# Optimization experiments

Measured on AMD Instinct MI355X. Metric: run time of the kernel, lower is better.

## Reference

```python
import jax, jax.numpy as jnp
import numpy as np

N, E, H, NH, D, T, L = 50000, 800000, 128, 8, 16, 6, 2  # nodes, edges, hidden, heads, head_dim, node types, layers


def setup_inputs() -> dict:
    key = jax.random.key(0)
    ks = jax.random.split(key, 16)
    s = 1.0 / np.sqrt(H)
    return {
        "hidden": jax.random.normal(ks[0], (N, H), jnp.float32),
        "cn": jax.random.normal(ks[1], (N, H), jnp.float32),
        "x_norm_abs": jax.random.uniform(ks[2], (N, 2), jnp.float32),
        "node_type": jax.random.randint(ks[3], (N,), 0, T, jnp.int32),
        "edge_src": jax.random.randint(ks[4], (E,), 0, N, jnp.int32),
        "edge_dst": jax.random.randint(ks[5], (E,), 0, N, jnp.int32),
        # learned params, stacked over L layers (num_relations=1 folded out)
        "W_pos": jax.random.normal(ks[6], (L, 2, H), jnp.float32) * 0.1,
        "Wk": jax.random.normal(ks[7], (L, T, H, H), jnp.float32) * s,
        "Wq": jax.random.normal(ks[8], (L, T, H, H), jnp.float32) * s,
        "Wv": jax.random.normal(ks[9], (L, T, H, H), jnp.float32) * s,
        "Wa": jax.random.normal(ks[10], (L, T, H, H), jnp.float32) * s,
        "rel_att": jax.random.normal(ks[11], (L, NH, D, D), jnp.float32) * (1.0 / np.sqrt(D)),
        "rel_msg": jax.random.normal(ks[12], (L, NH, D, D), jnp.float32) * (1.0 / np.sqrt(D)),
        "rel_pri": jnp.ones((L, NH), jnp.float32),
        "skip": jnp.zeros((L, T), jnp.float32),
        "w_pri": jax.random.normal(ks[13], (L, H), jnp.float32) * s,
    }


def reference(hidden, cn, x_norm_abs, node_type, edge_src, edge_dst,
              W_pos, Wk, Wq, Wv, Wa, rel_att, rel_msg, rel_pri, skip, w_pri):
    n, h_dim = hidden.shape
    nh, d = rel_att.shape[1], rel_att.shape[2]
    inv_sqrt_d = 1.0 / np.sqrt(d)
    ar = jnp.arange(n)
    priority = jnp.zeros((n,), hidden.dtype)

    for l in range(Wk.shape[0]):  # small fixed layer count
        h = hidden + x_norm_abs @ W_pos[l]                      # positional injection of x_norm_abs

        def per_type(W):
            all_t = jnp.einsum('nh,thd->tnd', h, W)             # [T,N,H] per-node-type projections
            return all_t[node_type, ar].reshape(n, nh, d)       # select own type -> [N,NH,D]

        k, q, v = per_type(Wk[l]), per_type(Wq[l]), per_type(Wv[l])
        ke, qe, ve = k[edge_src], q[edge_dst], v[edge_src]      # [E,NH,D] irregular gathers

        att = jnp.einsum('ehd,hdf,ehf->eh', ke, rel_att[l], qe) * rel_pri[l] * inv_sqrt_d
        amax = jax.ops.segment_max(att, edge_dst, num_segments=n)
        ex = jnp.exp(att - amax[edge_dst])
        den = jax.ops.segment_sum(ex, edge_dst, num_segments=n)
        alpha = ex / (den[edge_dst] + 1e-16)                    # per-destination softmax over edges

        msg = jnp.einsum('ehd,hdf->ehf', ve, rel_msg[l]) * alpha[..., None]
        agg = jax.ops.segment_sum(msg.reshape(-1, nh * d), edge_dst, num_segments=n)  # [N,H]

        trans = jax.nn.gelu(agg)
        out_all = jnp.einsum('nh,thd->tnd', trans, Wa[l])
        out = out_all[node_type, ar]
        sk = jax.nn.sigmoid(skip[l])[node_type][:, None]
        hgt_out = sk * out + (1.0 - sk) * h

        priority = jax.nn.sigmoid(hgt_out @ w_pri[l])
        cn = hgt_out + cn                                       # cn_now = hgt_out + cn_now
        hidden = hidden + jnp.tanh(cn)                          # hidden = hidden + tanh(cn)

    return hidden, cn, priority
```

## Files before the change

### kernel.cpp

```cpp
#include <hip/hip_runtime.h>
#include <hip/hip_bf16.h>
#include <math.h>

#define N_NODES 50000
#define N_EDGES 800000
#define HID     128
#define NHEAD   8
#define HDIM    16
#define NTYPE   6
#define NLAYER  2
#define TILE_N  64
#define PROJ_BLOCKS_PER_TYPE 782

typedef unsigned int uint_;
typedef unsigned short ushort_;

__device__ __forceinline__ float sigmoidf_(float x){ return 1.f/(1.f+__expf(-x)); }
__device__ __forceinline__ float gelu_tanh(float x){
  float x3 = x*x*x;
  return 0.5f*x*(1.f + tanhf(0.7978845608028654f*(x + 0.044715f*x3)));
}
__device__ __forceinline__ uint_ pack_bf2(float lo, float hi){
  union{float f; uint_ u;} a, b; a.f = lo; b.f = hi;
  uint_ ua = (a.u + 0x7FFFu + ((a.u >> 16) & 1u)) >> 16;
  uint_ ub = (b.u + 0x7FFFu + ((b.u >> 16) & 1u)) & 0xFFFF0000u;
  return ua | ub;
}

__global__ void k_hist(const int* __restrict__ edst, int* __restrict__ deg){
  int e = blockIdx.x*256 + threadIdx.x;
  if (e < N_EDGES) atomicAdd(&deg[edst[e]], 1);
}

__global__ void __launch_bounds__(1024)
k_scan(const int* __restrict__ deg, int* __restrict__ rowptr){
  __shared__ int part[1024];
  const int chunk = (N_NODES + 1023)/1024;
  int t = threadIdx.x;
  int beg = t*chunk, end = min(beg+chunk, N_NODES);
  int s = 0;
  for (int i = beg; i < end; ++i) s += deg[i];
  part[t] = s;
  __syncthreads();
  if (t == 0){
    int acc = 0;
    for (int i = 0; i < 1024; ++i){ int v = part[i]; part[i] = acc; acc += v; }
    rowptr[N_NODES] = acc;
  }
  __syncthreads();
  int acc = part[t];
  for (int i = beg; i < end; ++i){ rowptr[i] = acc; acc += deg[i]; }
}

__global__ void k_fill(const int* __restrict__ esrc, const int* __restrict__ edst,
                       const int* __restrict__ rowptr, int* __restrict__ cursor,
                       int* __restrict__ csr_src){
  int e = blockIdx.x*256 + threadIdx.x;
  if (e < N_EDGES){
    int d = edst[e];
    int pos = atomicAdd(&cursor[d], 1);
    csr_src[rowptr[d] + pos] = esrc[e];
  }
}

__global__ void k_thist(const int* __restrict__ ntype, int* __restrict__ tcount){
  __shared__ int c[NTYPE];
  int t = threadIdx.x;
  if (t < NTYPE) c[t] = 0;
  __syncthreads();
  int n = blockIdx.x*256 + t;
  if (n < N_NODES) atomicAdd(&c[ntype[n]], 1);
  __syncthreads();
  if (t < NTYPE && c[t] > 0) atomicAdd(&tcount[t], c[t]);
}

__global__ void k_tscan(const int* __restrict__ tcount, int* __restrict__ toffset){
  if (threadIdx.x == 0){
    int acc = 0;
    for (int i = 0; i < NTYPE; ++i){ toffset[i] = acc; acc += tcount[i]; }
  }
}

__global__ void k_tfill(const int* __restrict__ ntype, const int* __restrict__ toffset,
                        int* __restrict__ tcursor, int* __restrict__ tnodes){
  __shared__ int c[NTYPE], base[NTYPE];
  int t = threadIdx.x;
  if (t < NTYPE) c[t] = 0;
  __syncthreads();
  int n = blockIdx.x*256 + t;
  int ty = 0, rank = 0;
  bool valid = (n < N_NODES);
  if (valid){ ty = ntype[n]; rank = atomicAdd(&c[ty], 1); }
  __syncthreads();
  if (t < NTYPE && c[t] > 0) base[t] = atomicAdd(&tcursor[t], c[t]);
  __syncthreads();
  if (valid) tnodes[toffset[ty] + base[ty] + rank] = n;
}

__global__ void k_effw(const float* __restrict__ Wk, const float* __restrict__ Wv,
                       const float* __restrict__ A, const float* __restrict__ M,
                       const float* __restrict__ pri, float* __restrict__ WkA,
                       float* __restrict__ WvM){
  int idx = blockIdx.x*256 + threadIdx.x;
  if (idx >= NTYPE*HID*HID) return;
  int hf = idx & (HID-1);
  int hh = hf >> 4, f = hf & 15;
  int base = idx - hf;
  const float* a  = A + hh*HDIM*HDIM;
  const float* m  = M + hh*HDIM*HDIM;
  const float* wk = Wk + base + hh*HDIM;
  const float* wv = Wv + base + hh*HDIM;
  float sa = 0.f, sm = 0.f;
  #pragma unroll
  for (int d = 0; d < HDIM; ++d){ sa += wk[d]*a[d*HDIM+f]; sm += wv[d]*m[d*HDIM+f]; }
  WkA[idx] = sa * pri[hh] * 0.25f;
  WvM[idx] = sm;
}

__global__ void __launch_bounds__(256)
k_proj_t(const float* __restrict__ hidden, const float* __restrict__ xnorm,
         const int* __restrict__ tnodes, const int* __restrict__ tcount,
         const int* __restrict__ toffset, const float* __restrict__ Wpos,
         const float* __restrict__ Wq, const float* __restrict__ WkA,
         const float* __restrict__ WvM, float* __restrict__ qout,
         ushort_* __restrict__ kvout){
  int bid  = blockIdx.x;
  int m    = bid % 3;
  int rest = bid / 3;
  int ty   = rest / PROJ_BLOCKS_PER_TYPE;
  int tile = rest % PROJ_BLOCKS_PER_TYPE;
  int cnt  = tcount[ty];
  int base = tile*TILE_N;
  if (base >= cnt) return;
  __shared__ float hs[TILE_N][HID];
  __shared__ int nl[TILE_N];
  int t  = threadIdx.x;
  int c  = t & 31;
  int rt = t >> 5;
  int off = toffset[ty];
  float4 w0 = *(const float4*)(Wpos + 4*c);
  float4 w1 = *(const float4*)(Wpos + HID + 4*c);
  #pragma unroll
  for (int pass = 0; pass < 8; ++pass){
    int r = pass*8 + rt;
    int node = -1;
    float4 hv = make_float4(0.f,0.f,0.f,0.f);
    if (base + r < cnt){
      node = tnodes[off + base + r];
      float xa0 = xnorm[2*node], xa1 = xnorm[2*node+1];
      float4 hd = *(const float4*)(hidden + (size_t)node*HID + 4*c);
      hv.x = hd.x + xa0*w0.x + xa1*w1.x;
      hv.y = hd.y + xa0*w0.y + xa1*w1.y;
      hv.z = hd.z + xa0*w0.z + xa1*w1.z;
      hv.w = hd.w + xa0*w0.w + xa1*w1.w;
    }
    if (c == 0) nl[r] = node;
    *(float4*)&hs[r][4*c] = hv;
  }
  __syncthreads();

  const float* W = (m == 0 ? Wq : (m == 1 ? WkA : WvM)) + (size_t)ty*HID*HID;
  float4 acc[8];
  #pragma unroll
  for (int r = 0; r < 8; ++r) acc[r] = make_float4(0.f,0.f,0.f,0.f);
  for (int k0 = 0; k0 < HID; k0 += 4){
    float4 hr[8];
    #pragma unroll
    for (int r = 0; r < 8; ++r) hr[r] = *(const float4*)&hs[rt*8+r][k0];
    #pragma unroll
    for (int kk = 0; kk < 4; ++kk){
      float4 w = *(const float4*)(W + (size_t)(k0+kk)*HID + 4*c);
      #pragma unroll
      for (int r = 0; r < 8; ++r){
        float hvv = ((const float*)&hr[r])[kk];
        acc[r].x = fmaf(hvv, w.x, acc[r].x);
        acc[r].y = fmaf(hvv, w.y, acc[r].y);
        acc[r].z = fmaf(hvv, w.z, acc[r].z);
        acc[r].w = fmaf(hvv, w.w, acc[r].w);
      }
    }
  }
  #pragma unroll
  for (int r = 0; r < 8; ++r){
    int node = nl[rt*8+r];
    if (node >= 0){
      if (m == 0){
        *(float4*)(qout + (size_t)node*HID + 4*c) = acc[r];
      } else {
        uint2 pk = make_uint2(pack_bf2(acc[r].x, acc[r].y),
                              pack_bf2(acc[r].z, acc[r].w));
        size_t o = (size_t)node*2*HID + (m == 2 ? HID : 0) + 4*c;
        *(uint2*)(kvout + o) = pk;
      }
    }
  }
}

__global__ void k_edge(const int* __restrict__ rowptr, const int* __restrict__ csr_src,
                       const float* __restrict__ q, const ushort_* __restrict__ kv,
                       float* __restrict__ trans){
  int wid = threadIdx.x >> 6, lane = threadIdx.x & 63;
  int n = blockIdx.x*4 + wid;
  int j = 2*lane;
  int beg = rowptr[n], end = rowptr[n+1];
  float2 qv = *(const float2*)(q + (size_t)n*HID + j);
  float m = -INFINITY, s = 0.f, a0 = 0.f, a1 = 0.f;
  int e = beg;
  for (; e + 4 <= end; e += 4){
    uint_ kb[4], vb[4];
    float p[4];
    #pragma unroll
    for (int u = 0; u < 4; ++u){
      const ushort_* r0 = kv + (size_t)csr_src[e+u]*2*HID + j;
      kb[u] = *(const uint_*)r0;
      vb[u] = *(const uint_*)(r0 + HID);
    }
    #pragma unroll
    for (int u = 0; u < 4; ++u){
      float kx = __uint_as_float(kb[u] << 16);
      float ky = __uint_as_float(kb[u] & 0xFFFF0000u);
      float pp = kx*qv.x + ky*qv.y;
      pp += __shfl_xor(pp,1); pp += __shfl_xor(pp,2); pp += __shfl_xor(pp,4);
      p[u] = pp;
    }
    float mn = fmaxf(fmaxf(p[0],p[1]), fmaxf(p[2],p[3]));
    mn = fmaxf(m, mn);
    float fct = __expf(m - mn);
    s *= fct; a0 *= fct; a1 *= fct;
    #pragma unroll
    for (int u = 0; u < 4; ++u){
      float w = __expf(p[u] - mn);
      float vx = __uint_as_float(vb[u] << 16);
      float vy = __uint_as_float(vb[u] & 0xFFFF0000u);
      s += w; a0 = fmaf(w, vx, a0); a1 = fmaf(w, vy, a1);
    }
    m = mn;
  }
  for (; e < end; ++e){
    const ushort_* r0 = kv + (size_t)csr_src[e]*2*HID + j;
    uint_ kb = *(const uint_*)r0;
    uint_ vb = *(const uint_*)(r0 + HID);
    float kx = __uint_as_float(kb << 16);
    float ky = __uint_as_float(kb & 0xFFFF0000u);
    float pp = kx*qv.x + ky*qv.y;
    pp += __shfl_xor(pp,1); pp += __shfl_xor(pp,2); pp += __shfl_xor(pp,4);
    float mn  = fmaxf(m, pp);
    float fct = __expf(m - mn);
    float w   = __expf(pp - mn);
    float vx = __uint_as_float(vb << 16);
    float vy = __uint_as_float(vb & 0xFFFF0000u);
    s  = s*fct + w;
    a0 = fmaf(w, vx, a0*fct);
    a1 = fmaf(w, vy, a1*fct);
    m = mn;
  }
  float inv = 1.f/(s + 1e-16f);
  *(float2*)(trans + (size_t)n*HID + j) =
      make_float2(gelu_tanh(a0*inv), gelu_tanh(a1*inv));
}

__global__ void __launch_bounds__(256)
k_post_t(const float* __restrict__ trans, const float* __restrict__ xnorm,
         const int* __restrict__ tnodes, const int* __restrict__ tcount,
         const int* __restrict__ toffset, const float* __restrict__ Wpos,
         const float* __restrict__ Wa, const float* __restrict__ skip,
         const float* __restrict__ wpri,
         const float* __restrict__ hsrc, const float* __restrict__ csrc,
         float* __restrict__ hdst, float* __restrict__ cdst,
         float* __restrict__ pri, int last){
  int ty   = blockIdx.x / PROJ_BLOCKS_PER_TYPE;
  int tile = blockIdx.x % PROJ_BLOCKS_PER_TYPE;
  int cnt  = tcount[ty];
  int base = tile*TILE_N;
  if (base >= cnt) return;
  __shared__ float ts[TILE_N][HID];
  __shared__ int nl[TILE_N];
  int t  = threadIdx.x;
  int c  = t & 31;
  int rt = t >> 5;
  int off = toffset[ty];
  #pragma unroll
  for (int pass = 0; pass < 8; ++pass){
    int r = pass*8 + rt;
    int node = -1;
    float4 tv = make_float4(0.f,0.f,0.f,0.f);
    if (base + r < cnt){
      node = tnodes[off + base + r];
      tv = *(const float4*)(trans + (size_t)node*HID + 4*c);
    }
    if (c == 0) nl[r] = node;
    *(float4*)&ts[r][4*c] = tv;
  }
  __syncthreads();

  const float* W = Wa + (size_t)ty*HID*HID;
  float4 acc[8];
  #pragma unroll
  for (int r = 0; r < 8; ++r) acc[r] = make_float4(0.f,0.f,0.f,0.f);
  for (int k0 = 0; k0 < HID; k0 += 4){
    float4 hr[8];
    #pragma unroll
    for (int r = 0; r < 8; ++r) hr[r] = *(const float4*)&ts[rt*8+r][k0];
    #pragma unroll
    for (int kk = 0; kk < 4; ++kk){
      float4 w = *(const float4*)(W + (size_t)(k0+kk)*HID + 4*c);
      #pragma unroll
      for (int r = 0; r < 8; ++r){
        float hvv = ((const float*)&hr[r])[kk];
        acc[r].x = fmaf(hvv, w.x, acc[r].x);
        acc[r].y = fmaf(hvv, w.y, acc[r].y);
        acc[r].z = fmaf(hvv, w.z, acc[r].z);
        acc[r].w = fmaf(hvv, w.w, acc[r].w);
      }
    }
  }

  float sk = sigmoidf_(skip[ty]);
  float4 w0 = *(const float4*)(Wpos + 4*c);
  float4 w1 = *(const float4*)(Wpos + HID + 4*c);
  float4 wp = *(const float4*)(wpri + 4*c);
  float ppv[8];
  #pragma unroll
  for (int r = 0; r < 8; ++r){
    int node = nl[rt*8+r];
    ppv[r] = 0.f;
    if (node < 0) continue;
    size_t o = (size_t)node*HID + 4*c;
    float xa0 = xnorm[2*node], xa1 = xnorm[2*node+1];
    float4 hd = *(const float4*)(hsrc + o);
    float4 cv = *(const float4*)(csrc + o);
    float h0 = hd.x + xa0*w0.x + xa1*w1.x;
    float h1 = hd.y + xa0*w0.y + xa1*w1.y;
    float h2 = hd.z + xa0*w0.z + xa1*w1.z;
    float h3 = hd.w + xa0*w0.w + xa1*w1.w;
    float hg0 = sk*acc[r].x + (1.f - sk)*h0;
    float hg1 = sk*acc[r].y + (1.f - sk)*h1;
    float hg2 = sk*acc[r].z + (1.f - sk)*h2;
    float hg3 = sk*acc[r].w + (1.f - sk)*h3;
    ppv[r] = hg0*wp.x + hg1*wp.y + hg2*wp.z + hg3*wp.w;
    float c0 = hg0 + cv.x, c1 = hg1 + cv.y, c2 = hg2 + cv.z, c3 = hg3 + cv.w;
    *(float4*)(cdst + o) = make_float4(c0, c1, c2, c3);
    *(float4*)(hdst + o) = make_float4(hd.x + tanhf(c0), hd.y + tanhf(c1),
                                       hd.z + tanhf(c2), hd.w + tanhf(c3));
  }
  if (last){
    #pragma unroll
    for (int r = 0; r < 8; ++r){
      float pp = ppv[r];
      pp += __shfl_xor(pp, 1); pp += __shfl_xor(pp, 2); pp += __shfl_xor(pp, 4);
      pp += __shfl_xor(pp, 8); pp += __shfl_xor(pp, 16);
      ppv[r] = pp;
    }
    if (c == 0){
      #pragma unroll
      for (int r = 0; r < 8; ++r){
        int node = nl[rt*8+r];
        if (node >= 0) pri[node] = sigmoidf_(ppv[r]);
      }
    }
  }
}

extern "C" void kernel_launch(void* const* d_in, const int* in_sizes, int n_in,
                              void* d_out, int out_size, void* d_ws, size_t ws_size,
                              hipStream_t stream){
  const float* hidden_in = (const float*)d_in[0];
  const float* cn_in     = (const float*)d_in[1];
  const float* xnorm     = (const float*)d_in[2];
  const int*   ntype     = (const int*)d_in[3];
  const int*   esrc      = (const int*)d_in[4];
  const int*   edst      = (const int*)d_in[5];
  const float* Wpos      = (const float*)d_in[6];
  const float* Wk        = (const float*)d_in[7];
  const float* Wq        = (const float*)d_in[8];
  const float* Wv        = (const float*)d_in[9];
  const float* Wa        = (const float*)d_in[10];
  const float* Ratt      = (const float*)d_in[11];
  const float* Rmsg      = (const float*)d_in[12];
  const float* Rpri      = (const float*)d_in[13];
  const float* Skip      = (const float*)d_in[14];
  const float* Wpri      = (const float*)d_in[15];

  char* ws = (char*)d_ws;
  size_t off = 0;
  auto alloc = [&](size_t bytes)->void*{ void* p = ws + off; off += (bytes + 255) & ~(size_t)255; return p; };
  float*   qbuf  = (float*)alloc((size_t)N_NODES*HID*4);
  ushort_* kvbuf = (ushort_*)alloc((size_t)N_NODES*2*HID*2);
  float* WkA   = (float*)alloc((size_t)NTYPE*HID*HID*4);
  float* WvM   = (float*)alloc((size_t)NTYPE*HID*HID*4);
  int* deg     = (int*)alloc((size_t)N_NODES*4);
  int* rowptr  = (int*)alloc((size_t)(N_NODES+1)*4);
  int* cursor  = (int*)alloc((size_t)N_NODES*4);
  int* csr     = (int*)alloc((size_t)N_EDGES*4);
  int* tcount  = (int*)alloc(8*4);
  int* toffset = (int*)alloc(8*4);
  int* tcursor = (int*)alloc(8*4);
  int* tnodes  = (int*)alloc((size_t)N_NODES*4);

  float* out_hidden = (float*)d_out;
  float* out_cn     = out_hidden + (size_t)N_NODES*HID;
  float* out_pri    = out_cn     + (size_t)N_NODES*HID;

  hipMemsetAsync(deg,     0, (size_t)N_NODES*4, stream);
  hipMemsetAsync(cursor,  0, (size_t)N_NODES*4, stream);
  hipMemsetAsync(tcount,  0, 8*4, stream);
  hipMemsetAsync(tcursor, 0, 8*4, stream);
  k_hist<<<(N_EDGES+255)/256, 256, 0, stream>>>(edst, deg);
  k_scan<<<1, 1024, 0, stream>>>(deg, rowptr);
  k_fill<<<(N_EDGES+255)/256, 256, 0, stream>>>(esrc, edst, rowptr, cursor, csr);
  k_thist<<<(N_NODES+255)/256, 256, 0, stream>>>(ntype, tcount);
  k_tscan<<<1, 64, 0, stream>>>(tcount, toffset);
  k_tfill<<<(N_NODES+255)/256, 256, 0, stream>>>(ntype, toffset, tcursor, tnodes);

  const int proj_grid = 3 * NTYPE * PROJ_BLOCKS_PER_TYPE;
  const int post_grid = NTYPE * PROJ_BLOCKS_PER_TYPE;
  for (int l = 0; l < NLAYER; ++l){
    const float* Wpos_l = Wpos + (size_t)l*2*HID;
    const float* Wq_l   = Wq   + (size_t)l*NTYPE*HID*HID;
    const float* Wk_l   = Wk   + (size_t)l*NTYPE*HID*HID;
    const float* Wv_l   = Wv   + (size_t)l*NTYPE*HID*HID;
    const float* Wa_l   = Wa   + (size_t)l*NTYPE*HID*HID;
    const float* Ratt_l = Ratt + (size_t)l*NHEAD*HDIM*HDIM;
    const float* Rmsg_l = Rmsg + (size_t)l*NHEAD*HDIM*HDIM;
    const float* Rpri_l = Rpri + (size_t)l*NHEAD;
    const float* Skip_l = Skip + (size_t)l*NTYPE;
    const float* Wpri_l = Wpri + (size_t)l*HID;

    const float* hsrc = (l == 0) ? hidden_in : out_hidden;
    const float* csrc = (l == 0) ? cn_in     : out_cn;

    k_effw<<<(NTYPE*HID*HID+255)/256, 256, 0, stream>>>(Wk_l, Wv_l, Ratt_l, Rmsg_l, Rpri_l, WkA, WvM);
    k_proj_t<<<proj_grid, 256, 0, stream>>>(hsrc, xnorm, tnodes, tcount, toffset,
                                            Wpos_l, Wq_l, WkA, WvM, qbuf, kvbuf);
    k_edge<<<N_NODES/4, 256, 0, stream>>>(rowptr, csr, qbuf, kvbuf, qbuf);
    k_post_t<<<post_grid, 256, 0, stream>>>(qbuf, xnorm, tnodes, tcount, toffset,
                                            Wpos_l, Wa_l, Skip_l, Wpri_l,
                                            hsrc, csrc, out_hidden, out_cn,
                                            out_pri, l == NLAYER-1);
  }
}
```

Measured before the change: 675.9 us.

## Use bf16 MFMA for per-type projection and output GEMMs with prepacked weights

Replaces the scalar FP32 shared-memory GEMMs in the projection and post kernels with bf16 MFMA 16x16x32 instructions. A new weight-pack kernel folds the relation matrices into Wk and Wv, converts all four weight sets to bf16, and stores them in MFMA fragment order. The projection kernel now does q, k and v in one block, so activations are loaded once instead of three times. The risks are reduced precision from bf16 inputs and more scattered, narrower stores (per-element writes across node rows) in place of float4 writes.

```diff
diff --git a/kernel.cpp b/kernel.cpp
--- a/kernel.cpp
+++ b/kernel.cpp
@@ -9,22 +9,21 @@
 #define HDIM    16
 #define NTYPE   6
 #define NLAYER  2
-#define TILE_N  64
-#define PROJ_BLOCKS_PER_TYPE 782
+#define PBT     782
 
 typedef unsigned int uint_;
 typedef unsigned short ushort_;
+typedef __attribute__((ext_vector_type(4))) float f32x4;
+typedef __attribute__((ext_vector_type(8))) short short8;
 
 __device__ __forceinline__ float sigmoidf_(float x){ return 1.f/(1.f+__expf(-x)); }
 __device__ __forceinline__ float gelu_tanh(float x){
   float x3 = x*x*x;
   return 0.5f*x*(1.f + tanhf(0.7978845608028654f*(x + 0.044715f*x3)));
 }
-__device__ __forceinline__ uint_ pack_bf2(float lo, float hi){
-  union{float f; uint_ u;} a, b; a.f = lo; b.f = hi;
-  uint_ ua = (a.u + 0x7FFFu + ((a.u >> 16) & 1u)) >> 16;
-  uint_ ub = (b.u + 0x7FFFu + ((b.u >> 16) & 1u)) & 0xFFFF0000u;
-  return ua | ub;
+__device__ __forceinline__ ushort_ bf16r(float x){
+  union{float f; uint_ u;} v; v.f = x;
+  return (ushort_)((v.u + 0x7FFFu + ((v.u >> 16) & 1u)) >> 16);
 }
 
 __global__ void k_hist(const int* __restrict__ edst, int* __restrict__ deg){
@@ -97,100 +96,113 @@
   if (valid) tnodes[toffset[ty] + base[ty] + rank] = n;
 }
 
-__global__ void k_effw(const float* __restrict__ Wk, const float* __restrict__ Wv,
-                       const float* __restrict__ A, const float* __restrict__ M,
-                       const float* __restrict__ pri, float* __restrict__ WkA,
-                       float* __restrict__ WvM){
+__global__ void k_packw(const float* __restrict__ Wq, const float* __restrict__ Wk,
+                        const float* __restrict__ Wv, const float* __restrict__ Wa,
+                        const float* __restrict__ A,  const float* __restrict__ M,
+                        const float* __restrict__ pri, uint4* __restrict__ wpk){
   int idx = blockIdx.x*256 + threadIdx.x;
-  if (idx >= NTYPE*HID*HID) return;
-  int hf = idx & (HID-1);
-  int hh = hf >> 4, f = hf & 15;
-  int base = idx - hf;
-  const float* a  = A + hh*HDIM*HDIM;
-  const float* m  = M + hh*HDIM*HDIM;
-  const float* wk = Wk + base + hh*HDIM;
-  const float* wv = Wv + base + hh*HDIM;
-  float sa = 0.f, sm = 0.f;
-  #pragma unroll
-  for (int d = 0; d < HDIM; ++d){ sa += wk[d]*a[d*HDIM+f]; sm += wv[d]*m[d*HDIM+f]; }
-  WkA[idx] = sa * pri[hh] * 0.25f;
-  WvM[idx] = sm;
+  if (idx >= NTYPE*4*4*8*64) return;
+  int l  = idx & 63;
+  int ct = (idx >> 6) & 7;
+  int ks = (idx >> 9) & 3;
+  int m  = (idx >> 11) & 3;
+  int t  = idx >> 13;
+  int kbase = ks*32 + (l >> 4)*8;
+  int c15 = l & 15;
+  ushort_ out[8];
+  if (m == 0 || m == 3){
+    const float* W = (m == 0 ? Wq : Wa) + (size_t)t*HID*HID;
+    int col = ct*16 + c15;
+    #pragma unroll
+    for (int j = 0; j < 8; ++j) out[j] = bf16r(W[(size_t)(kbase+j)*HID + col]);
+  } else {
+    const float* W = (m == 1 ? Wk : Wv) + (size_t)t*HID*HID;
+    const float* R = (m == 1 ? A : M) + ct*HDIM*HDIM;
+    float scale = (m == 1) ? pri[ct]*0.25f : 1.f;
+    #pragma unroll
+    for (int j = 0; j < 8; ++j){
+      const float* wrow = W + (size_t)(kbase+j)*HID + ct*16;
+      float s = 0.f;
+      #pragma unroll
+      for (int d = 0; d < HDIM; ++d) s += wrow[d]*R[d*HDIM + c15];
+      out[j] = bf16r(s*scale);
+    }
+  }
+  uint4 pk;
+  pk.x = (uint_)out[0] | ((uint_)out[1] << 16);
+  pk.y = (uint_)out[2] | ((uint_)out[3] << 16);
+  pk.z = (uint_)out[4] | ((uint_)out[5] << 16);
+  pk.w = (uint_)out[6] | ((uint_)out[7] << 16);
+  wpk[idx] = pk;
 }
 
 __global__ void __launch_bounds__(256)
-k_proj_t(const float* __restrict__ hidden, const float* __restrict__ xnorm,
+k_proj_t(const float* __restrict__ hsrc, const float* __restrict__ xnorm,
          const int* __restrict__ tnodes, const int* __restrict__ tcount,
          const int* __restrict__ toffset, const float* __restrict__ Wpos,
-         const float* __restrict__ Wq, const float* __restrict__ WkA,
-         const float* __restrict__ WvM, float* __restrict__ qout,
+         const uint4* __restrict__ wpk, float* __restrict__ qout,
          ushort_* __restrict__ kvout){
-  int bid  = blockIdx.x;
-  int m    = bid % 3;
-  int rest = bid / 3;
-  int ty   = rest / PROJ_BLOCKS_PER_TYPE;
-  int tile = rest % PROJ_BLOCKS_PER_TYPE;
+  int ty   = blockIdx.x / PBT;
+  int tile = blockIdx.x % PBT;
   int cnt  = tcount[ty];
-  int base = tile*TILE_N;
-  if (base >= cnt) return;
-  __shared__ float hs[TILE_N][HID];
-  __shared__ int nl[TILE_N];
-  int t  = threadIdx.x;
-  int c  = t & 31;
-  int rt = t >> 5;
+  int wid  = threadIdx.x >> 6, l = threadIdx.x & 63;
+  int rowbase = tile*64 + wid*16;
+  if (rowbase >= cnt) return;
   int off = toffset[ty];
-  float4 w0 = *(const float4*)(Wpos + 4*c);
-  float4 w1 = *(const float4*)(Wpos + HID + 4*c);
+  int l15 = l & 15, lk = l >> 4;
+
+  int nrowA = rowbase + l15;
+  int nodeA = tnodes[off + (nrowA < cnt ? nrowA : 0)];
+  float xa0 = xnorm[2*nodeA], xa1 = xnorm[2*nodeA+1];
+  short8 afr[4];
   #pragma unroll
-  for (int pass = 0; pass < 8; ++pass){
-    int r = pass*8 + rt;
-    int node = -1;
-    float4 hv = make_float4(0.f,0.f,0.f,0.f);
-    if (base + r < cnt){
-      node = tnodes[off + base + r];
-      float xa0 = xnorm[2*node], xa1 = xnorm[2*node+1];
-      float4 hd = *(const float4*)(hidden + (size_t)node*HID + 4*c);
-      hv.x = hd.x + xa0*w0.x + xa1*w1.x;
-      hv.y = hd.y + xa0*w0.y + xa1*w1.y;
-      hv.z = hd.z + xa0*w0.z + xa1*w1.z;
-      hv.w = hd.w + xa0*w0.w + xa1*w1.w;
-    }
-    if (c == 0) nl[r] = node;
-    *(float4*)&hs[r][4*c] = hv;
-  }
-  __syncthreads();
-
-  const float* W = (m == 0 ? Wq : (m == 1 ? WkA : WvM)) + (size_t)ty*HID*HID;
-  float4 acc[8];
+  for (int ks = 0; ks < 4; ++ks){
+    int col = ks*32 + lk*8;
+    float4 h0 = *(const float4*)(hsrc + (size_t)nodeA*HID + col);
+    float4 h1 = *(const float4*)(hsrc + (size_t)nodeA*HID + col + 4);
+    float4 p0 = *(const float4*)(Wpos + col);
+    float4 p1 = *(const float4*)(Wpos + col + 4);
+    float4 q0 = *(const float4*)(Wpos + HID + col);
+    float4 q1 = *(const float4*)(Wpos + HID + col + 4);
+    union{ ushort_ h[8]; short8 s; } ap;
+    ap.h[0] = bf16r(h0.x + xa0*p0.x + xa1*q0.x);
+    ap.h[1] = bf16r(h0.y + xa0*p0.y + xa1*q0.y);
+    ap.h[2] = bf16r(h0.z + xa0*p0.z + xa1*q0.z);
+    ap.h[3] = bf16r(h0.w + xa0*p0.w + xa1*q0.w);
+    ap.h[4] = bf16r(h1.x + xa0*p1.x + xa1*q1.x);
+    ap.h[5] = bf16r(h1.y + xa0*p1.y + xa1*q1.y);
+    ap.h[6] = bf16r(h1.z + xa0*p1.z + xa1*q1.z);
+    ap.h[7] = bf16r(h1.w + xa0*p1.w + xa1*q1.w);
+    afr[ks] = ap.s;
+  }
+
+  int  ndw[4]; bool nvw[4];
   #pragma unroll
-  for (int r = 0; r < 8; ++r) acc[r] = make_float4(0.f,0.f,0.f,0.f);
-  for (int k0 = 0; k0 < HID; k0 += 4){
-    float4 hr[8];
-    #pragma unroll
-    for (int r = 0; r < 8; ++r) hr[r] = *(const float4*)&hs[rt*8+r][k0];
-    #pragma unroll
-    for (int kk = 0; kk < 4; ++kk){
-      float4 w = *(const float4*)(W + (size_t)(k0+kk)*HID + 4*c);
+  for (int reg = 0; reg < 4; ++reg){
+    int nr = rowbase + lk*4 + reg;
+    nvw[reg] = (nr < cnt);
+    ndw[reg] = tnodes[off + (nvw[reg] ? nr : 0)];
+  }
+
+  #pragma unroll 1
+  for (int m = 0; m < 3; ++m){
+    const uint4* wb = wpk + ((size_t)(ty*4 + m)*32)*64;
+    #pragma unroll 1
+    for (int ct = 0; ct < 8; ++ct){
+      f32x4 acc = {0.f, 0.f, 0.f, 0.f};
       #pragma unroll
-      for (int r = 0; r < 8; ++r){
-        float hvv = ((const float*)&hr[r])[kk];
-        acc[r].x = fmaf(hvv, w.x, acc[r].x);
-        acc[r].y = fmaf(hvv, w.y, acc[r].y);
-        acc[r].z = fmaf(hvv, w.z, acc[r].z);
-        acc[r].w = fmaf(hvv, w.w, acc[r].w);
+      for (int ks = 0; ks < 4; ++ks){
+        union{ uint4 u; short8 s; } bw;
+        bw.u = wb[(ks*8 + ct)*64 + l];
+        acc = __builtin_amdgcn_mfma_f32_16x16x32_bf16(afr[ks], bw.s, acc, 0, 0, 0);
       }
-    }
-  }
-  #pragma unroll
-  for (int r = 0; r < 8; ++r){
-    int node = nl[rt*8+r];
-    if (node >= 0){
-      if (m == 0){
-        *(float4*)(qout + (size_t)node*HID + 4*c) = acc[r];
-      } else {
-        uint2 pk = make_uint2(pack_bf2(acc[r].x, acc[r].y),
-                              pack_bf2(acc[r].z, acc[r].w));
-        size_t o = (size_t)node*2*HID + (m == 2 ? HID : 0) + 4*c;
-        *(uint2*)(kvout + o) = pk;
+      int colw = ct*16 + l15;
+      #pragma unroll
+      for (int reg = 0; reg < 4; ++reg){
+        if (nvw[reg]){
+          if (m == 0) qout[(size_t)ndw[reg]*HID + colw] = acc[reg];
+          else kvout[(size_t)ndw[reg]*2*HID + (m == 2 ? HID : 0) + colw] = bf16r(acc[reg]);
+        }
       }
     }
   }
@@ -263,100 +275,77 @@
 k_post_t(const float* __restrict__ trans, const float* __restrict__ xnorm,
          const int* __restrict__ tnodes, const int* __restrict__ tcount,
          const int* __restrict__ toffset, const float* __restrict__ Wpos,
-         const float* __restrict__ Wa, const float* __restrict__ skip,
+         const uint4* __restrict__ wpk, const float* __restrict__ skip,
          const float* __restrict__ wpri,
          const float* __restrict__ hsrc, const float* __restrict__ csrc,
          float* __restrict__ hdst, float* __restrict__ cdst,
          float* __restrict__ pri, int last){
-  int ty   = blockIdx.x / PROJ_BLOCKS_PER_TYPE;
-  int tile = blockIdx.x % PROJ_BLOCKS_PER_TYPE;
+  int ty   = blockIdx.x / PBT;
+  int tile = blockIdx.x % PBT;
   int cnt  = tcount[ty];
-  int base = tile*TILE_N;
-  if (base >= cnt) return;
-  __shared__ float ts[TILE_N][HID];
-  __shared__ int nl[TILE_N];
-  int t  = threadIdx.x;
-  int c  = t & 31;
-  int rt = t >> 5;
+  int wid  = threadIdx.x >> 6, l = threadIdx.x & 63;
+  int rowbase = tile*64 + wid*16;
+  if (rowbase >= cnt) return;
   int off = toffset[ty];
+  int l15 = l & 15, lk = l >> 4;
+
+  int nrowA = rowbase + l15;
+  int nodeA = tnodes[off + (nrowA < cnt ? nrowA : 0)];
+  short8 afr[4];
   #pragma unroll
-  for (int pass = 0; pass < 8; ++pass){
-    int r = pass*8 + rt;
-    int node = -1;
-    float4 tv = make_float4(0.f,0.f,0.f,0.f);
-    if (base + r < cnt){
-      node = tnodes[off + base + r];
-      tv = *(const float4*)(trans + (size_t)node*HID + 4*c);
-    }
-    if (c == 0) nl[r] = node;
-    *(float4*)&ts[r][4*c] = tv;
-  }
-  __syncthreads();
-
-  const float* W = Wa + (size_t)ty*HID*HID;
-  float4 acc[8];
-  #pragma unroll
-  for (int r = 0; r < 8; ++r) acc[r] = make_float4(0.f,0.f,0.f,0.f);
-  for (int k0 = 0; k0 < HID; k0 += 4){
-    float4 hr[8];
-    #pragma unroll
-    for (int r = 0; r < 8; ++r) hr[r] = *(const float4*)&ts[rt*8+r][k0];
-    #pragma unroll
-    for (int kk = 0; kk < 4; ++kk){
-      float4 w = *(const float4*)(W + (size_t)(k0+kk)*HID + 4*c);
-      #pragma unroll
-      for (int r = 0; r < 8; ++r){
-        float hvv = ((const float*)&hr[r])[kk];
-        acc[r].x = fmaf(hvv, w.x, acc[r].x);
-        acc[r].y = fmaf(hvv, w.y, acc[r].y);
-        acc[r].z = fmaf(hvv, w.z, acc[r].z);
-        acc[r].w = fmaf(hvv, w.w, acc[r].w);
+  for (int ks = 0; ks < 4; ++ks){
+    int col = ks*32 + lk*8;
+    float4 t0 = *(const float4*)(trans + (size_t)nodeA*HID + col);
+    float4 t1 = *(const float4*)(trans + (size_t)nodeA*HID + col + 4);
+    union{ ushort_ h[8]; short8 s; } ap;
+    ap.h[0] = bf16r(t0.x); ap.h[1] = bf16r(t0.y);
+    ap.h[2] = bf16r(t0.z); ap.h[3] = bf16r(t0.w);
+    ap.h[4] = bf16r(t1.x); ap.h[5] = bf16r(t1.y);
+    ap.h[6] = bf16r(t1.z); ap.h[7] = bf16r(t1.w);
+    afr[ks] = ap.s;
+  }
+
+  const uint4* wb = wpk + ((size_t)(ty*4 + 3)*32)*64;
+  f32x4 accs[8];
+  #pragma unroll 1
+  for (int ct = 0; ct < 8; ++ct){
+    f32x4 acc = {0.f, 0.f, 0.f, 0.f};
+    #pragma unroll
+    for (int ks = 0; ks < 4; ++ks){
+      union{ uint4 u; short8 s; } bw;
+      bw.u = wb[(ks*8 + ct)*64 + l];
+      acc = __builtin_amdgcn_mfma_f32_16x16x32_bf16(afr[ks], bw.s, acc, 0, 0, 0);
+    }
+    accs[ct] = acc;
+  }
+
+  float sk = sigmoidf_(skip[ty]);
+  #pragma unroll 1
+  for (int reg = 0; reg < 4; ++reg){
+    int nr = rowbase + lk*4 + reg;
+    bool nv = (nr < cnt);
+    int nd = tnodes[off + (nv ? nr : 0)];
+    float xa0 = xnorm[2*nd], xa1 = xnorm[2*nd+1];
+    float ppart = 0.f;
+    #pragma unroll
+    for (int ct = 0; ct < 8; ++ct){
+      int col = ct*16 + l15;
+      size_t o = (size_t)nd*HID + col;
+      float w0 = Wpos[col], w1 = Wpos[HID + col];
+      float hd = hsrc[o];
+      float h  = hd + xa0*w0 + xa1*w1;
+      float hg = sk*accs[ct][reg] + (1.f - sk)*h;
+      if (last) ppart = fmaf(hg, wpri[col], ppart);
+      float cnew = hg + csrc[o];
+      if (nv){
+        cdst[o] = cnew;
+        hdst[o] = hd + tanhf(cnew);
       }
     }
-  }
-
-  float sk = sigmoidf_(skip[ty]);
-  float4 w0 = *(const float4*)(Wpos + 4*c);
-  float4 w1 = *(const float4*)(Wpos + HID + 4*c);
-  float4 wp = *(const float4*)(wpri + 4*c);
-  float ppv[8];
-  #pragma unroll
-  for (int r = 0; r < 8; ++r){
-    int node = nl[rt*8+r];
-    ppv[r] = 0.f;
-    if (node < 0) continue;
-    size_t o = (size_t)node*HID + 4*c;
-    float xa0 = xnorm[2*node], xa1 = xnorm[2*node+1];
-    float4 hd = *(const float4*)(hsrc + o);
-    float4 cv = *(const float4*)(csrc + o);
-    float h0 = hd.x + xa0*w0.x + xa1*w1.x;
-    float h1 = hd.y + xa0*w0.y + xa1*w1.y;
-    float h2 = hd.z + xa0*w0.z + xa1*w1.z;
-    float h3 = hd.w + xa0*w0.w + xa1*w1.w;
-    float hg0 = sk*acc[r].x + (1.f - sk)*h0;
-    float hg1 = sk*acc[r].y + (1.f - sk)*h1;
-    float hg2 = sk*acc[r].z + (1.f - sk)*h2;
-    float hg3 = sk*acc[r].w + (1.f - sk)*h3;
-    ppv[r] = hg0*wp.x + hg1*wp.y + hg2*wp.z + hg3*wp.w;
-    float c0 = hg0 + cv.x, c1 = hg1 + cv.y, c2 = hg2 + cv.z, c3 = hg3 + cv.w;
-    *(float4*)(cdst + o) = make_float4(c0, c1, c2, c3);
-    *(float4*)(hdst + o) = make_float4(hd.x + tanhf(c0), hd.y + tanhf(c1),
-                                       hd.z + tanhf(c2), hd.w + tanhf(c3));
-  }
-  if (last){
-    #pragma unroll
-    for (int r = 0; r < 8; ++r){
-      float pp = ppv[r];
-      pp += __shfl_xor(pp, 1); pp += __shfl_xor(pp, 2); pp += __shfl_xor(pp, 4);
-      pp += __shfl_xor(pp, 8); pp += __shfl_xor(pp, 16);
-      ppv[r] = pp;
-    }
-    if (c == 0){
-      #pragma unroll
-      for (int r = 0; r < 8; ++r){
-        int node = nl[rt*8+r];
-        if (node >= 0) pri[node] = sigmoidf_(ppv[r]);
-      }
+    if (last){
+      ppart += __shfl_xor(ppart, 1); ppart += __shfl_xor(ppart, 2);
+      ppart += __shfl_xor(ppart, 4); ppart += __shfl_xor(ppart, 8);
+      if (l15 == 0 && nv) pri[nd] = sigmoidf_(ppart);
     }
   }
 }
@@ -386,8 +375,7 @@
   auto alloc = [&](size_t bytes)->void*{ void* p = ws + off; off += (bytes + 255) & ~(size_t)255; return p; };
   float*   qbuf  = (float*)alloc((size_t)N_NODES*HID*4);
   ushort_* kvbuf = (ushort_*)alloc((size_t)N_NODES*2*HID*2);
-  float* WkA   = (float*)alloc((size_t)NTYPE*HID*HID*4);
-  float* WvM   = (float*)alloc((size_t)NTYPE*HID*HID*4);
+  uint4*   wpk   = (uint4*)alloc((size_t)NTYPE*4*4*8*64*16);
   int* deg     = (int*)alloc((size_t)N_NODES*4);
   int* rowptr  = (int*)alloc((size_t)(N_NODES+1)*4);
   int* cursor  = (int*)alloc((size_t)N_NODES*4);
@@ -412,8 +400,7 @@
   k_tscan<<<1, 64, 0, stream>>>(tcount, toffset);
   k_tfill<<<(N_NODES+255)/256, 256, 0, stream>>>(ntype, toffset, tcursor, tnodes);
 
-  const int proj_grid = 3 * NTYPE * PROJ_BLOCKS_PER_TYPE;
-  const int post_grid = NTYPE * PROJ_BLOCKS_PER_TYPE;
+  const int gemm_grid = NTYPE * PBT;
   for (int l = 0; l < NLAYER; ++l){
     const float* Wpos_l = Wpos + (size_t)l*2*HID;
     const float* Wq_l   = Wq   + (size_t)l*NTYPE*HID*HID;
@@ -429,12 +416,13 @@
     const float* hsrc = (l == 0) ? hidden_in : out_hidden;
     const float* csrc = (l == 0) ? cn_in     : out_cn;
 
-    k_effw<<<(NTYPE*HID*HID+255)/256, 256, 0, stream>>>(Wk_l, Wv_l, Ratt_l, Rmsg_l, Rpri_l, WkA, WvM);
-    k_proj_t<<<proj_grid, 256, 0, stream>>>(hsrc, xnorm, tnodes, tcount, toffset,
-                                            Wpos_l, Wq_l, WkA, WvM, qbuf, kvbuf);
+    k_packw<<<(NTYPE*4*4*8*64 + 255)/256, 256, 0, stream>>>(
+        Wq_l, Wk_l, Wv_l, Wa_l, Ratt_l, Rmsg_l, Rpri_l, wpk);
+    k_proj_t<<<gemm_grid, 256, 0, stream>>>(hsrc, xnorm, tnodes, tcount, toffset,
+                                            Wpos_l, wpk, qbuf, kvbuf);
     k_edge<<<N_NODES/4, 256, 0, stream>>>(rowptr, csr, qbuf, kvbuf, qbuf);
-    k_post_t<<<post_grid, 256, 0, stream>>>(qbuf, xnorm, tnodes, tcount, toffset,
-                                            Wpos_l, Wa_l, Skip_l, Wpri_l,
+    k_post_t<<<gemm_grid, 256, 0, stream>>>(qbuf, xnorm, tnodes, tcount, toffset,
+                                            Wpos_l, wpk, Skip_l, Wpri_l,
                                             hsrc, csrc, out_hidden, out_cn,
                                             out_pri, l == NLAYER-1);
   }
```

Result: faster. 602.8 us (-10.8%).
